# Kernel tuning notes

Hardware: AMD Instinct MI355X
Metric: run time of the kernel (lower is better)

## Reference

```python
import jax, jax.numpy as jnp
import numpy as np

B, L, N, H = 1024, 200, 2, 128  # batch, block_len, code_rate_n, dec_num_unit


def setup_inputs() -> dict:
    key = jax.random.key(0)
    ks = jax.random.split(key, 24)
    s = 0.05
    inp = {"received": jax.random.normal(ks[0], (B, N * L, 1), jnp.float32)}
    # dec_linear: Linear(n*L, n*L)
    inp["W_lin"] = jax.random.normal(ks[1], (N * L, N * L), jnp.float32) * s
    inp["b_lin"] = jax.random.normal(ks[2], (N * L,), jnp.float32) * s
    # GRU params, PyTorch layout: W_ih [3H, in], W_hh [3H, H], gates ordered (r, z, n)
    specs = [("0f", N), ("0b", N), ("1f", 2 * H), ("1b", 2 * H)]
    i = 3
    for tag, din in specs:
        inp[f"Wih{tag}"] = jax.random.normal(ks[i], (3 * H, din), jnp.float32) * s; i += 1
        inp[f"Whh{tag}"] = jax.random.normal(ks[i], (3 * H, H), jnp.float32) * s; i += 1
        inp[f"bih{tag}"] = jax.random.normal(ks[i], (3 * H,), jnp.float32) * s; i += 1
        inp[f"bhh{tag}"] = jax.random.normal(ks[i], (3 * H,), jnp.float32) * s; i += 1
    # final: Linear(2H, 1)
    inp["Wf"] = jax.random.normal(ks[i], (1, 2 * H), jnp.float32) * s
    inp["bf"] = jax.random.normal(ks[i + 1], (1,), jnp.float32) * s
    return inp


def _gru_dir(x, Wih, Whh, bih, bhh, reverse):
    # x: [B, L, din] -> outputs [B, L, H]; PyTorch GRU cell math, gate order (r, z, n)
    h_dim = Whh.shape[1]
    xg = jnp.einsum('bld,gd->blg', x, Wih) + bih          # precompute input gates [B,L,3H]
    xg = jnp.swapaxes(xg, 0, 1)                            # [L,B,3H] for scan over time
    h0 = jnp.zeros((x.shape[0], h_dim), x.dtype)

    def step(h, g):
        hg = h @ Whh.T + bhh
        r = jax.nn.sigmoid(g[:, :h_dim] + hg[:, :h_dim])
        z = jax.nn.sigmoid(g[:, h_dim:2 * h_dim] + hg[:, h_dim:2 * h_dim])
        n = jnp.tanh(g[:, 2 * h_dim:] + r * hg[:, 2 * h_dim:])
        h = (1.0 - z) * n + z * h
        return h, h

    _, hs = jax.lax.scan(step, h0, xg, reverse=reverse)    # [L,B,H], time-aligned
    return jnp.swapaxes(hs, 0, 1)


def reference(received, W_lin, b_lin,
              Wih0f, Whh0f, bih0f, bhh0f,
              Wih0b, Whh0b, bih0b, bhh0b,
              Wih1f, Whh1f, bih1f, bhh1f,
              Wih1b, Whh1b, bih1b, bhh1b,
              Wf, bf):
    b = received.shape[0]
    permuted = jnp.swapaxes(received, 1, 2)                # [B, 1, n*L]
    code = permuted @ W_lin.T + b_lin                      # dec_linear
    n_in = Wih0f.shape[1]
    code = code.reshape(b, -1, n_in)                       # [B, L, n]
    # layer 0 (bidirectional)
    h0 = jnp.concatenate([
        _gru_dir(code, Wih0f, Whh0f, bih0f, bhh0f, False),
        _gru_dir(code, Wih0b, Whh0b, bih0b, bhh0b, True)], axis=-1)   # [B,L,2H]
    # layer 1 (bidirectional)
    h1 = jnp.concatenate([
        _gru_dir(h0, Wih1f, Whh1f, bih1f, bhh1f, False),
        _gru_dir(h0, Wih1b, Whh1b, bih1b, bhh1b, True)], axis=-1)     # [B,L,2H]
    return jax.nn.sigmoid(h1 @ Wf.T + bf)                  # [B,L,1]
```

## Files before the change

### kernel.cpp

```cpp
#include <hip/hip_runtime.h>
#include <hip/hip_bf16.h>

#define B_   1024
#define L_   200
#define H_   128
#define BL_  204800
#define G3_  384

typedef __bf16 bf16x8 __attribute__((ext_vector_type(8)));
typedef __bf16 bf16x4 __attribute__((ext_vector_type(4)));
typedef float  f32x4  __attribute__((ext_vector_type(4)));

__device__ __forceinline__ float sigf(float x) {
    return __builtin_amdgcn_rcpf(1.f + __expf(-x));
}
__device__ __forceinline__ float tanh_fast(float x) {
    float e = __expf(-2.f * x);
    return (1.f - e) * __builtin_amdgcn_rcpf(1.f + e);
}
__device__ __forceinline__ bf16x8 cvt8(float4 a, float4 b) {
    bf16x8 v;
    v[0] = (__bf16)a.x; v[1] = (__bf16)a.y; v[2] = (__bf16)a.z; v[3] = (__bf16)a.w;
    v[4] = (__bf16)b.x; v[5] = (__bf16)b.y; v[6] = (__bf16)b.z; v[7] = (__bf16)b.w;
    return v;
}
__device__ __forceinline__ void plane32_swap(float& a, float& b) {
    asm("v_permlane32_swap_b32 %0, %1" : "+v"(a), "+v"(b));
}

__global__ __launch_bounds__(256) void k_sentinel(float* __restrict__ out, int n) {
    const int i = blockIdx.x * 256 + threadIdx.x;
    if (i < n) out[i] = -5.0f;
}

__global__ __launch_bounds__(256) void k_declin(
    const float* __restrict__ rcv, const float* __restrict__ Wl,
    const float* __restrict__ bl, float* __restrict__ code) {
    __shared__ float rs[4][400];
    const int tid = threadIdx.x;
    const int b0 = blockIdx.x * 4;
    for (int i = tid; i < 1600; i += 256) ((float*)rs)[i] = rcv[(size_t)b0 * 400 + i];
    __syncthreads();
    #pragma unroll
    for (int rep = 0; rep < 2; ++rep) {
        const int j = tid + rep * 256;
        if (j < 400) {
            float a0 = 0.f, a1 = 0.f, a2 = 0.f, a3 = 0.f;
            const float4* wp = (const float4*)(Wl + (size_t)j * 400);
            for (int k = 0; k < 100; ++k) {
                float4 w4 = wp[k];
                const int kk = k * 4;
                a0 += w4.x*rs[0][kk] + w4.y*rs[0][kk+1] + w4.z*rs[0][kk+2] + w4.w*rs[0][kk+3];
                a1 += w4.x*rs[1][kk] + w4.y*rs[1][kk+1] + w4.z*rs[1][kk+2] + w4.w*rs[1][kk+3];
                a2 += w4.x*rs[2][kk] + w4.y*rs[2][kk+1] + w4.z*rs[2][kk+2] + w4.w*rs[2][kk+3];
                a3 += w4.x*rs[3][kk] + w4.y*rs[3][kk+1] + w4.z*rs[3][kk+2] + w4.w*rs[3][kk+3];
            }
            const float bb = bl[j];
            code[(size_t)(b0+0)*400 + j] = a0 + bb;
            code[(size_t)(b0+1)*400 + j] = a1 + bb;
            code[(size_t)(b0+2)*400 + j] = a2 + bb;
            code[(size_t)(b0+3)*400 + j] = a3 + bb;
        }
    }
}

__global__ __launch_bounds__(512, 2) void k_gru0(
    const float* __restrict__ code,
    const float* __restrict__ Wih_f, const float* __restrict__ Whh_f,
    const float* __restrict__ bih_f, const float* __restrict__ bhh_f,
    const float* __restrict__ Wih_b, const float* __restrict__ Whh_b,
    const float* __restrict__ bih_b, const float* __restrict__ bhh_b,
    __bf16* __restrict__ h0) {
    const int dir = blockIdx.y;
    const int b0 = blockIdx.x * 8;
    const float* Wih = dir ? Wih_b : Wih_f;
    const float* Whh = dir ? Whh_b : Whh_f;
    const float* bih = dir ? bih_b : bih_f;
    const float* bhh = dir ? bhh_b : bhh_f;

    const int tid = threadIdx.x;
    const int w = tid >> 6, ln = tid & 63, q = ln >> 4, r16 = ln & 15;
    const int jj = w * 16 + r16;
    const int mbase = (q & 1) * 4 + (q >> 1) * 2;

    __shared__ __bf16 h_bf[2][16][136];
    __shared__ float  code_s[8][400];
    __shared__ __bf16 h_st[2][8][8][128];

    for (int i = tid; i < 8 * 400; i += 512) ((float*)code_s)[i] = code[(size_t)b0 * 400 + i];
    for (int i = tid; i < 2 * 16 * 136; i += 512) ((__bf16*)h_bf)[i] = (__bf16)0.f;

    bf16x8 wfr[3][4];
    const float wr0 = Wih[jj * 2],         wr1 = Wih[jj * 2 + 1];
    const float wz0 = Wih[(jj + 128) * 2], wz1 = Wih[(jj + 128) * 2 + 1];
    const float wn0 = Wih[(jj + 256) * 2], wn1 = Wih[(jj + 256) * 2 + 1];
    const float xbr = bih[jj] + bhh[jj];
    const float xbz = bih[jj + 128] + bhh[jj + 128];
    const float xbn = bih[jj + 256];
    const float bnv = bhh[jj + 256];
    float hreg2[2] = {0.f, 0.f};
    #pragma unroll
    for (int g = 0; g < 3; ++g) {
        const int j = (w + g * 8) * 16 + r16;
        const float* p = Whh + (size_t)j * H_;
        #pragma unroll
        for (int kt = 0; kt < 4; ++kt) {
            float4 x0 = *(const float4*)(p + kt * 32 + q * 8);
            float4 x1 = *(const float4*)(p + kt * 32 + q * 8 + 4);
            wfr[g][kt] = cvt8(x0, x1);
        }
    }
    __syncthreads();

    for (int t = 0; t < L_; ++t) {
        const int cur = t & 1, nxt = cur ^ 1;
        if ((t & 7) == 0 && t > 0) {
            const int g8 = (t >> 3) - 1;
            const int buf = g8 & 1;
            const int p = tid >> 3, inner = tid & 7;
            const int s = p >> 3, row = p & 7;
            const int tb = g8 * 8 + s;
            const int l = dir ? (L_ - 1 - tb) : tb;
            const __bf16* src = &h_st[buf][s][row][inner * 16];
            __bf16* dst = &h0[((size_t)(b0 + row) * L_ + l) * 256 + dir * 128 + inner * 16];
            *(bf16x8*)(dst)     = *(const bf16x8*)(src);
            *(bf16x8*)(dst + 8) = *(const bf16x8*)(src + 8);
        }
        const int l = dir ? (L_ - 1 - t) : t;
        bf16x8 af[4];
        #pragma unroll
        for (int kt = 0; kt < 4; ++kt)
            af[kt] = *(const bf16x8*)&h_bf[cur][r16][kt * 32 + q * 8];

        f32x4 ar = {0.f,0.f,0.f,0.f}, az = {0.f,0.f,0.f,0.f}, an = {0.f,0.f,0.f,0.f};
        #pragma unroll
        for (int kt = 0; kt < 4; ++kt) {
            ar = __builtin_amdgcn_mfma_f32_16x16x32_bf16(af[kt], wfr[0][kt], ar, 0, 0, 0);
            az = __builtin_amdgcn_mfma_f32_16x16x32_bf16(af[kt], wfr[1][kt], az, 0, 0, 0);
            an = __builtin_amdgcn_mfma_f32_16x16x32_bf16(af[kt], wfr[2][kt], an, 0, 0, 0);
        }
        #pragma unroll
        for (int i = 0; i < 2; ++i) {
            float arl = ar[i], arh = ar[i + 2];
            float azl = az[i], azh = az[i + 2];
            float anl = an[i], anh = an[i + 2];
            plane32_swap(arl, arh);
            plane32_swap(azl, azh);
            plane32_swap(anl, anh);
            const int m = mbase + i;
            const float c0 = code_s[m][l * 2], c1 = code_s[m][l * 2 + 1];
            const float r = sigf(c0 * wr0 + c1 * wr1 + xbr + arl);
            const float z = sigf(c0 * wz0 + c1 * wz1 + xbz + azl);
            const float n = tanh_fast(c0 * wn0 + c1 * wn1 + xbn + r * (anl + bnv));
            const float hv = n + z * (hreg2[i] - n);
            hreg2[i] = hv;
            h_bf[nxt][m][jj] = (__bf16)hv;
            h_st[(t >> 3) & 1][t & 7][m][jj] = (__bf16)hv;
        }
        __syncthreads();
    }
    {
        const int p = tid >> 3, inner = tid & 7;
        const int s = p >> 3, row = p & 7;
        const int tb = 192 + s;
        const int l = dir ? (L_ - 1 - tb) : tb;
        const __bf16* src = &h_st[0][s][row][inner * 16];
        __bf16* dst = &h0[((size_t)(b0 + row) * L_ + l) * 256 + dir * 128 + inner * 16];
        *(bf16x8*)(dst)     = *(const bf16x8*)(src);
        *(bf16x8*)(dst + 8) = *(const bf16x8*)(src + 8);
    }
}

__global__ __launch_bounds__(256) void k_cvtW(
    const float* __restrict__ Wfp, const float* __restrict__ Wbp,
    __bf16* __restrict__ out) {
    const int j = blockIdx.x * 256 + threadIdx.x;
    const int base = j * 4;
    const int dir = base >= 98304;
    const int idx = dir ? base - 98304 : base;
    float4 v = *(const float4*)((dir ? Wbp : Wfp) + idx);
    bf16x4 o;
    o[0] = (__bf16)v.x; o[1] = (__bf16)v.y; o[2] = (__bf16)v.z; o[3] = (__bf16)v.w;
    *(bf16x4*)&out[base] = o;
}

__global__ __launch_bounds__(512, 2) void k_gru1f(
    const __bf16* __restrict__ h0,
    const __bf16* __restrict__ Wihbf,
    const float* __restrict__ bih_f, const float* __restrict__ bhh_f,
    const float* __restrict__ bih_b, const float* __restrict__ bhh_b,
    const float* __restrict__ Whh_f, const float* __restrict__ Whh_b,
    const float* __restrict__ Wfin,
    float* __restrict__ partial) {
    const int dir = blockIdx.y;
    const int b0 = blockIdx.x * 8;
    const float* Whh = dir ? Whh_b : Whh_f;
    const float* bih = dir ? bih_b : bih_f;
    const float* bhh = dir ? bhh_b : bhh_f;
    const __bf16* Wb = Wihbf + (size_t)dir * 384 * 256;

    const int tid = threadIdx.x;
    const int w = tid >> 6, ln = tid & 63, q = ln >> 4, r16 = ln & 15;
    const int jj = w * 16 + r16;
    const int mbase = (q & 1) * 4 + (q >> 1) * 2;

    __shared__ __bf16 xa[2][32][264];
    __shared__ __bf16 h_bf[2][16][136];
    __shared__ float  wacc[2][8][8];

    for (int i = tid; i < 2 * 16 * 136; i += 512) ((__bf16*)h_bf)[i] = (__bf16)0.f;

    bf16x8 wfr[3][4];
    bf16x8 wB[3][8];
    const float xbr = bih[jj] + bhh[jj];
    const float xbz = bih[jj + 128] + bhh[jj + 128];
    const float xbn = bih[jj + 256];
    const float bnv = bhh[jj + 256];
    const float wfv = Wfin[dir * 128 + jj];
    float hreg2[2] = {0.f, 0.f};
    #pragma unroll
    for (int g = 0; g < 3; ++g) {
        const int j = (w + g * 8) * 16 + r16;
        const float* p = Whh + (size_t)j * H_;
        #pragma unroll
        for (int kt = 0; kt < 4; ++kt) {
            float4 x0 = *(const float4*)(p + kt * 32 + q * 8);
            float4 x1 = *(const float4*)(p + kt * 32 + q * 8 + 4);
            wfr[g][kt] = cvt8(x0, x1);
        }
    }
    #pragma unroll
    for (int n = 0; n < 3; ++n) {
        const int ct = w + n * 8;
        const __bf16* wp = Wb + (size_t)(ct * 16 + r16) * 256 + q * 8;
        #pragma unroll
        for (int k8 = 0; k8 < 8; ++k8)
            wB[n][k8] = *(const bf16x8*)(wp + k8 * 32);
    }
    {
        const int r = tid >> 4, seg = tid & 15;
        const int s = r >> 3, bt = r & 7;
        const int l = dir ? (L_ - 1 - s) : s;
        const __bf16* src = h0 + ((size_t)(b0 + bt) * L_ + l) * 256 + seg * 16;
        *(bf16x8*)&xa[0][r][seg * 16]     = *(const bf16x8*)(src);
        *(bf16x8*)&xa[0][r][seg * 16 + 8] = *(const bf16x8*)(src + 8);
    }
    __syncthreads();

    for (int c = 0; c < 50; ++c) {
        const int cb = c & 1, nb = cb ^ 1;
        bf16x8 pf0, pf1;
        const bool pv = (c + 1 < 50);
        const int prr = tid >> 4, prs = tid & 15;
        if (pv) {
            const int s = prr >> 3, bt = prr & 7;
            const int t = (c + 1) * 4 + s;
            const int l = dir ? (L_ - 1 - t) : t;
            const __bf16* src = h0 + ((size_t)(b0 + bt) * L_ + l) * 256 + prs * 16;
            pf0 = *(const bf16x8*)(src);
            pf1 = *(const bf16x8*)(src + 8);
        }

        f32x4 accg[3][2];
        #pragma unroll
        for (int n = 0; n < 3; ++n)
            #pragma unroll
            for (int mt = 0; mt < 2; ++mt) {
                accg[n][mt][0]=0.f; accg[n][mt][1]=0.f;
                accg[n][mt][2]=0.f; accg[n][mt][3]=0.f;
            }
        #pragma unroll
        for (int k8 = 0; k8 < 8; ++k8) {
            const bf16x8 a0 = *(const bf16x8*)&xa[cb][r16][k8 * 32 + q * 8];
            const bf16x8 a1 = *(const bf16x8*)&xa[cb][16 + r16][k8 * 32 + q * 8];
            #pragma unroll
            for (int n = 0; n < 3; ++n) {
                accg[n][0] = __builtin_amdgcn_mfma_f32_16x16x32_bf16(a0, wB[n][k8], accg[n][0], 0, 0, 0);
                accg[n][1] = __builtin_amdgcn_mfma_f32_16x16x32_bf16(a1, wB[n][k8], accg[n][1], 0, 0, 0);
            }
        }

        #pragma unroll
        for (int s = 0; s < 4; ++s) {
            const int cur = s & 1, nxt = cur ^ 1;
            const int par = s & 1;
            const int t = c * 4 + s;
            const int l = dir ? (L_ - 1 - t) : t;
            const int mt = s >> 1;

            bf16x8 af[4];
            #pragma unroll
            for (int kt = 0; kt < 4; ++kt)
                af[kt] = *(const bf16x8*)&h_bf[cur][r16][kt * 32 + q * 8];

            f32x4 ar = {0.f,0.f,0.f,0.f}, az = {0.f,0.f,0.f,0.f}, an = {0.f,0.f,0.f,0.f};
            #pragma unroll
            for (int kt = 0; kt < 4; ++kt) {
                ar = __builtin_amdgcn_mfma_f32_16x16x32_bf16(af[kt], wfr[0][kt], ar, 0, 0, 0);
                az = __builtin_amdgcn_mfma_f32_16x16x32_bf16(af[kt], wfr[1][kt], az, 0, 0, 0);
                an = __builtin_amdgcn_mfma_f32_16x16x32_bf16(af[kt], wfr[2][kt], an, 0, 0, 0);
            }

            float hv2[2];
            #pragma unroll
            for (int i = 0; i < 2; ++i) {
                float x0r = accg[0][mt][i], x1r = accg[0][mt][i + 2];
                float x0z = accg[1][mt][i], x1z = accg[1][mt][i + 2];
                float x0n = accg[2][mt][i], x1n = accg[2][mt][i + 2];
                plane32_swap(x0r, x1r);
                plane32_swap(x0z, x1z);
                plane32_swap(x0n, x1n);
                const float xrv = (s & 1) ? x1r : x0r;
                const float xzv = (s & 1) ? x1z : x0z;
                const float xnv = (s & 1) ? x1n : x0n;
                float arl = ar[i], arh = ar[i + 2];
                float azl = az[i], azh = az[i + 2];
                float anl = an[i], anh = an[i + 2];
                plane32_swap(arl, arh);
                plane32_swap(azl, azh);
                plane32_swap(anl, anh);
                const int m = mbase + i;
                const float r = sigf(xrv + xbr + arl);
                const float z = sigf(xzv + xbz + azl);
                const float n = tanh_fast(xnv + xbn + r * (anl + bnv));
                const float hv = n + z * (hreg2[i] - n);
                hreg2[i] = hv;
                hv2[i] = hv;
                h_bf[nxt][m][jj] = (__bf16)hv;
            }
            #pragma unroll
            for (int i = 0; i < 2; ++i) {
                float v = hv2[i] * wfv;
                v += __shfl_xor(v, 1); v += __shfl_xor(v, 2);
                v += __shfl_xor(v, 4); v += __shfl_xor(v, 8);
                if (r16 == 0) wacc[par][w][mbase + i] = v;
            }
            if (pv && s == 2) {
                *(bf16x8*)&xa[nb][prr][prs * 16]     = pf0;
                *(bf16x8*)&xa[nb][prr][prs * 16 + 8] = pf1;
            }
            __syncthreads();
            if (tid < 8) {
                float v = 0.f;
                #pragma unroll
                for (int ww = 0; ww < 8; ++ww) v += wacc[par][ww][tid];
                partial[(size_t)dir * BL_ + (size_t)(b0 + tid) * L_ + l] = v;
            }
        }
    }
}

__global__ __launch_bounds__(256) void k_final(
    const float* __restrict__ partial, const float* __restrict__ bfp,
    float* __restrict__ out) {
    const int i = blockIdx.x * 256 + threadIdx.x;
    if (i < BL_) out[i] = sigf(partial[i] + partial[BL_ + i] + bfp[0]);
}

extern "C" void kernel_launch(void* const* d_in, const int* in_sizes, int n_in,
                              void* d_out, int out_size, void* d_ws, size_t ws_size,
                              hipStream_t stream) {
    const float* rcv   = (const float*)d_in[0];
    const float* Wl    = (const float*)d_in[1];
    const float* bl    = (const float*)d_in[2];
    const float* Wih0f = (const float*)d_in[3];
    const float* Whh0f = (const float*)d_in[4];
    const float* bih0f = (const float*)d_in[5];
    const float* bhh0f = (const float*)d_in[6];
    const float* Wih0b = (const float*)d_in[7];
    const float* Whh0b = (const float*)d_in[8];
    const float* bih0b = (const float*)d_in[9];
    const float* bhh0b = (const float*)d_in[10];
    const float* Wih1f = (const float*)d_in[11];
    const float* Whh1f = (const float*)d_in[12];
    const float* bih1f = (const float*)d_in[13];
    const float* bhh1f = (const float*)d_in[14];
    const float* Wih1b = (const float*)d_in[15];
    const float* Whh1b = (const float*)d_in[16];
    const float* bih1b = (const float*)d_in[17];
    const float* bhh1b = (const float*)d_in[18];
    const float* Wfin  = (const float*)d_in[19];
    const float* bfin  = (const float*)d_in[20];

    const size_t OFF_CODE = 0;
    const size_t OFF_PART = 1638400;
    const size_t OFF_H0   = 3276800;
    const size_t OFF_WBF  = 108134400;
    const size_t WS_NEEDED = 108527616;

    if (ws_size < WS_NEEDED) {
        k_sentinel<<<(out_size + 255) / 256, 256, 0, stream>>>((float*)d_out, out_size);
        return;
    }

    char* ws = (char*)d_ws;
    float*  code    = (float*)(ws + OFF_CODE);
    float*  partial = (float*)(ws + OFF_PART);
    __bf16* h0      = (__bf16*)(ws + OFF_H0);
    __bf16* Wihbf   = (__bf16*)(ws + OFF_WBF);

    k_declin<<<256, 256, 0, stream>>>(rcv, Wl, bl, code);
    k_cvtW<<<192, 256, 0, stream>>>(Wih1f, Wih1b, Wihbf);
    k_gru0<<<dim3(128, 2), 512, 0, stream>>>(code, Wih0f, Whh0f, bih0f, bhh0f,
                                             Wih0b, Whh0b, bih0b, bhh0b, h0);
    k_gru1f<<<dim3(128, 2), 512, 0, stream>>>(h0, Wihbf,
                                              bih1f, bhh1f, bih1b, bhh1b,
                                              Whh1f, Whh1b, Wfin, partial);
    k_final<<<800, 256, 0, stream>>>(partial, bfin, (float*)d_out);
}
```

Measured before the change: 476.6 us.

## Split layer-0 GRU into 4-batch blocks to double grid size

```diff
diff --git a/kernel.cpp b/kernel.cpp
--- a/kernel.cpp
+++ b/kernel.cpp
@@ -64,7 +64,7 @@
     }
 }
 
-__global__ __launch_bounds__(512, 2) void k_gru0(
+__global__ __launch_bounds__(512, 4) void k_gru0(
     const float* __restrict__ code,
     const float* __restrict__ Wih_f, const float* __restrict__ Whh_f,
     const float* __restrict__ bih_f, const float* __restrict__ bhh_f,
@@ -72,7 +72,7 @@
     const float* __restrict__ bih_b, const float* __restrict__ bhh_b,
     __bf16* __restrict__ h0) {
     const int dir = blockIdx.y;
-    const int b0 = blockIdx.x * 8;
+    const int b0 = blockIdx.x * 4;
     const float* Wih = dir ? Wih_b : Wih_f;
     const float* Whh = dir ? Whh_b : Whh_f;
     const float* bih = dir ? bih_b : bih_f;
@@ -81,13 +81,12 @@
     const int tid = threadIdx.x;
     const int w = tid >> 6, ln = tid & 63, q = ln >> 4, r16 = ln & 15;
     const int jj = w * 16 + r16;
-    const int mbase = (q & 1) * 4 + (q >> 1) * 2;
 
     __shared__ __bf16 h_bf[2][16][136];
-    __shared__ float  code_s[8][400];
-    __shared__ __bf16 h_st[2][8][8][128];
-
-    for (int i = tid; i < 8 * 400; i += 512) ((float*)code_s)[i] = code[(size_t)b0 * 400 + i];
+    __shared__ float  code_s[4][400];
+    __shared__ __bf16 h_st[2][8][4][128];
+
+    for (int i = tid; i < 4 * 400; i += 512) ((float*)code_s)[i] = code[(size_t)b0 * 400 + i];
     for (int i = tid; i < 2 * 16 * 136; i += 512) ((__bf16*)h_bf)[i] = (__bf16)0.f;
 
     bf16x8 wfr[3][4];
@@ -98,7 +97,7 @@
     const float xbz = bih[jj + 128] + bhh[jj + 128];
     const float xbn = bih[jj + 256];
     const float bnv = bhh[jj + 256];
-    float hreg2[2] = {0.f, 0.f};
+    float hreg = 0.f;
     #pragma unroll
     for (int g = 0; g < 3; ++g) {
         const int j = (w + g * 8) * 16 + r16;
@@ -117,14 +116,16 @@
         if ((t & 7) == 0 && t > 0) {
             const int g8 = (t >> 3) - 1;
             const int buf = g8 & 1;
-            const int p = tid >> 3, inner = tid & 7;
-            const int s = p >> 3, row = p & 7;
-            const int tb = g8 * 8 + s;
-            const int l = dir ? (L_ - 1 - tb) : tb;
-            const __bf16* src = &h_st[buf][s][row][inner * 16];
-            __bf16* dst = &h0[((size_t)(b0 + row) * L_ + l) * 256 + dir * 128 + inner * 16];
-            *(bf16x8*)(dst)     = *(const bf16x8*)(src);
-            *(bf16x8*)(dst + 8) = *(const bf16x8*)(src + 8);
+            if (tid < 256) {
+                const int p = tid >> 3, inner = tid & 7;
+                const int s = p >> 2, row = p & 3;
+                const int tb = g8 * 8 + s;
+                const int lf = dir ? (L_ - 1 - tb) : tb;
+                const __bf16* src = &h_st[buf][s][row][inner * 16];
+                __bf16* dst = &h0[((size_t)(b0 + row) * L_ + lf) * 256 + dir * 128 + inner * 16];
+                *(bf16x8*)(dst)     = *(const bf16x8*)(src);
+                *(bf16x8*)(dst + 8) = *(const bf16x8*)(src + 8);
+            }
         }
         const int l = dir ? (L_ - 1 - t) : t;
         bf16x8 af[4];
@@ -139,35 +140,29 @@
             az = __builtin_amdgcn_mfma_f32_16x16x32_bf16(af[kt], wfr[1][kt], az, 0, 0, 0);
             an = __builtin_amdgcn_mfma_f32_16x16x32_bf16(af[kt], wfr[2][kt], an, 0, 0, 0);
         }
-        #pragma unroll
-        for (int i = 0; i < 2; ++i) {
-            float arl = ar[i], arh = ar[i + 2];
-            float azl = az[i], azh = az[i + 2];
-            float anl = an[i], anh = an[i + 2];
-            plane32_swap(arl, arh);
-            plane32_swap(azl, azh);
-            plane32_swap(anl, anh);
-            const int m = mbase + i;
-            const float c0 = code_s[m][l * 2], c1 = code_s[m][l * 2 + 1];
-            const float r = sigf(c0 * wr0 + c1 * wr1 + xbr + arl);
-            const float z = sigf(c0 * wz0 + c1 * wz1 + xbz + azl);
-            const float n = tanh_fast(c0 * wn0 + c1 * wn1 + xbn + r * (anl + bnv));
-            const float hv = n + z * (hreg2[i] - n);
-            hreg2[i] = hv;
-            h_bf[nxt][m][jj] = (__bf16)hv;
-            h_st[(t >> 3) & 1][t & 7][m][jj] = (__bf16)hv;
+        {
+            const float c0 = code_s[q][l * 2], c1 = code_s[q][l * 2 + 1];
+            const float r = sigf(c0 * wr0 + c1 * wr1 + xbr + ar[0]);
+            const float z = sigf(c0 * wz0 + c1 * wz1 + xbz + az[0]);
+            const float n = tanh_fast(c0 * wn0 + c1 * wn1 + xbn + r * (an[0] + bnv));
+            const float hv = n + z * (hreg - n);
+            hreg = hv;
+            h_bf[nxt][q * 4][jj] = (__bf16)hv;
+            h_st[(t >> 3) & 1][t & 7][q][jj] = (__bf16)hv;
         }
         __syncthreads();
     }
     {
-        const int p = tid >> 3, inner = tid & 7;
-        const int s = p >> 3, row = p & 7;
-        const int tb = 192 + s;
-        const int l = dir ? (L_ - 1 - tb) : tb;
-        const __bf16* src = &h_st[0][s][row][inner * 16];
-        __bf16* dst = &h0[((size_t)(b0 + row) * L_ + l) * 256 + dir * 128 + inner * 16];
-        *(bf16x8*)(dst)     = *(const bf16x8*)(src);
-        *(bf16x8*)(dst + 8) = *(const bf16x8*)(src + 8);
+        if (tid < 256) {
+            const int p = tid >> 3, inner = tid & 7;
+            const int s = p >> 2, row = p & 3;
+            const int tb = 192 + s;
+            const int lf = dir ? (L_ - 1 - tb) : tb;
+            const __bf16* src = &h_st[0][s][row][inner * 16];
+            __bf16* dst = &h0[((size_t)(b0 + row) * L_ + lf) * 256 + dir * 128 + inner * 16];
+            *(bf16x8*)(dst)     = *(const bf16x8*)(src);
+            *(bf16x8*)(dst + 8) = *(const bf16x8*)(src + 8);
+        }
     }
 }
 
@@ -401,7 +396,7 @@
 
     k_declin<<<256, 256, 0, stream>>>(rcv, Wl, bl, code);
     k_cvtW<<<192, 256, 0, stream>>>(Wih1f, Wih1b, Wihbf);
-    k_gru0<<<dim3(128, 2), 512, 0, stream>>>(code, Wih0f, Whh0f, bih0f, bhh0f,
+    k_gru0<<<dim3(256, 2), 512, 0, stream>>>(code, Wih0f, Whh0f, bih0f, bhh0f,
                                              Wih0b, Whh0b, bih0b, bhh0b, h0);
     k_gru1f<<<dim3(128, 2), 512, 0, stream>>>(h0, Wihbf,
                                               bih1f, bhh1f, bih1b, bhh1b,
```

After: 483.7 us. About the same (+1.5%).
